# Kernel optimization log

Measured on AMD Instinct MI355X. Metric: run time of the kernel, lower is better.

Reference implementation:

```python
import jax, jax.numpy as jnp
import numpy as np

T_SCHEDULE = 999.0
LOG_2PI = float(np.log(2.0 * np.pi))


def setup_inputs() -> dict:
    key = jax.random.key(0)
    k1, k2, k3 = jax.random.split(key, 3)
    xt = jax.random.normal(k1, (128, 3, 32, 32), dtype=jnp.float32)
    # integer-style diffusion timesteps in [0, 900); divided by t_schedule=999 inside
    t = jax.random.uniform(k2, (128,), dtype=jnp.float32) * 900.0
    gt_images = jax.random.normal(k3, (20000, 3, 32, 32), dtype=jnp.float32)
    return {"xt": xt, "t": t, "gt_images": gt_images}


def reference(xt, t, gt_images):
    # AnalyticFlow.forward_fast
    B = xt.shape[0]
    N = gt_images.shape[0]
    x = jax.lax.stop_gradient(xt.reshape(B, -1))  # original detaches x
    gt = gt_images.reshape(N, -1)                 # [N, D]
    D = x.shape[-1]
    tt = t / T_SCHEDULE                           # [B]
    sig = 1.0 - tt                                # [B]
    # log N(term_2; 0, I) summed over D, where term_2 = (x - t*gt)/(1-t).
    # ||x - t*gt||^2 = ||x||^2 - 2 t x.gt + t^2 ||gt||^2  (avoids B*N*D tensor)
    x2 = jnp.sum(x * x, axis=-1)                  # [B]
    g2 = jnp.sum(gt * gt, axis=-1)                # [N]
    xg = x @ gt.T                                 # [B, N] GEMM
    sq = x2[:, None] - 2.0 * tt[:, None] * xg + (tt * tt)[:, None] * g2[None, :]
    log_p = -0.5 * sq / (sig * sig)[:, None] - 0.5 * D * LOG_2PI  # [B, N]
    log_p = log_p - jnp.max(log_p)                # global-max shift as in original
    eta = jax.nn.softmax(log_p, axis=1)           # [B, N], rows sum to 1
    # drift = mean_n (N*eta_n) * (gt_n - x)/(1-t) = (eta @ gt - x)/(1-t)
    drift = (eta @ gt - x) / sig[:, None]         # [B, D]
    return drift.reshape(xt.shape)
```

## Files before the change

kernel.cpp:

```cpp
#include <hip/hip_runtime.h>
#include <hip/hip_bf16.h>
#include <stdint.h>

#define B_SZ   128
#define D_SZ   3072
#define N_SZ   20000
#define NPAD   20480
#define BN     (B_SZ * NPAD)
#define BD     (B_SZ * D_SZ)

typedef __attribute__((ext_vector_type(8))) short        short8;
typedef __attribute__((ext_vector_type(4))) float        f32x4;
typedef __attribute__((ext_vector_type(2))) unsigned int uint2v;

__device__ __forceinline__ unsigned short f2bf(float f) {
    unsigned u = __float_as_uint(f);
    u += 0x7FFFu + ((u >> 16) & 1u);
    return (unsigned short)(u >> 16);
}
__device__ __forceinline__ float bf2f(unsigned short h) {
    return __uint_as_float(((unsigned)h) << 16);
}
__device__ __forceinline__ unsigned pk2bf(float a, float b) {
    __hip_bfloat162 h = __float22bfloat162_rn(make_float2(a, b));
    unsigned r;
    __builtin_memcpy(&r, &h, 4);
    return r;
}
__device__ __forceinline__ unsigned fkey_enc(float f) {
    unsigned b = __float_as_uint(f);
    return (b & 0x80000000u) ? ~b : (b | 0x80000000u);
}
__device__ __forceinline__ float fkey_dec(unsigned u) {
    return __uint_as_float((u & 0x80000000u) ? (u ^ 0x80000000u) : ~u);
}

__device__ __forceinline__ void gl_lds16(const void* g, void* l) {
    __builtin_amdgcn_global_load_lds(
        (const __attribute__((address_space(1))) void*)g,
        (__attribute__((address_space(3))) void*)l, 16, 0, 0);
}

__device__ __forceinline__ int swz(int r, int q) { return q ^ ((r >> 1) & 3); }

__global__ __launch_bounds__(256) void zero_small(float* __restrict__ p)
{
    p[blockIdx.x * 256 + threadIdx.x] = 0.f;
}

__global__ __launch_bounds__(256) void prep_x(const float* __restrict__ x,
                                              unsigned short* __restrict__ xhi,
                                              unsigned short* __restrict__ xlo)
{
    int i = blockIdx.x * 256 + threadIdx.x;
    float v = x[i];
    unsigned short h = f2bf(v);
    xhi[i] = h;
    xlo[i] = f2bf(v - bf2f(h));
}

__global__ __launch_bounds__(256) void scores_kernel(
        const float* __restrict__ gt,
        const unsigned short* __restrict__ xhi,
        const unsigned short* __restrict__ xlo,
        float* __restrict__ XG_part,
        float* __restrict__ G2)
{
    __shared__ __align__(16) unsigned short Xhi_t[128 * 32];
    __shared__ __align__(16) unsigned short Xlo_t[128 * 32];
    __shared__ __align__(16) unsigned short Ghi_t[64 * 32];
    __shared__ __align__(16) unsigned short Glo_t[64 * 32];

    const int tid   = threadIdx.x;
    const int kc    = blockIdx.x & 7;
    const int nt    = blockIdx.x >> 3;
    const int nbase = nt * 64;
    const int kcb   = kc * 384;

    const int lane = tid & 63;
    const int wave = tid >> 6;
    const int mh = wave & 1;
    const int nh = wave >> 1;
    const int lm = lane & 15;
    const int qd = lane >> 4;

    const int gn = tid >> 2;
    const int gq = tid & 3;
    const int ng0 = nbase + gn;
    int grow = ng0 > N_SZ - 1 ? N_SZ - 1 : ng0;
    const float* gp0 = gt + (size_t)grow * D_SZ + kcb + gq * 8;
    const int gwr = gn * 32 + swz(gn, gq) * 8;

    int xsrc[2], xdst[2];
    #pragma unroll
    for (int i = 0; i < 2; i++) {
        int o = (i * 256 + tid) * 16;
        int r = o >> 6;
        int j = (o >> 4) & 3;
        xdst[i] = o;
        xsrc[i] = r * D_SZ + kcb + swz(r, j) * 8;
    }

    float g2acc = 0.0f;

    f32x4 acc[4][2];
    #pragma unroll
    for (int i = 0; i < 4; i++)
        #pragma unroll
        for (int j = 0; j < 2; j++)
            acc[i][j] = (f32x4){0.f, 0.f, 0.f, 0.f};

    for (int k0 = 0; k0 < 384; k0 += 32) {
        #pragma unroll
        for (int i = 0; i < 2; i++) {
            gl_lds16(xhi + xsrc[i] + k0, (char*)Xhi_t + xdst[i]);
            gl_lds16(xlo + xsrc[i] + k0, (char*)Xlo_t + xdst[i]);
        }
        f32x4 v0 = *(const f32x4*)(gp0 + k0);
        f32x4 v1 = *(const f32x4*)(gp0 + k0 + 4);
        short8 h8, l8;
        #pragma unroll
        for (int j = 0; j < 4; j++) {
            float a = v0[j], b = v1[j];
            unsigned short ha = f2bf(a), hb = f2bf(b);
            h8[j]     = (short)ha;  h8[j + 4] = (short)hb;
            l8[j]     = (short)f2bf(a - bf2f(ha));
            l8[j + 4] = (short)f2bf(b - bf2f(hb));
            g2acc += a * a + b * b;
        }
        *(short8*)&Ghi_t[gwr] = h8;
        *(short8*)&Glo_t[gwr] = l8;

        __syncthreads();

        short8 bhi[2], blo[2];
        #pragma unroll
        for (int ni = 0; ni < 2; ni++) {
            int r = nh * 32 + ni * 16 + lm;
            int sl = r * 32 + swz(r, qd) * 8;
            bhi[ni] = *(short8*)&Ghi_t[sl];
            blo[ni] = *(short8*)&Glo_t[sl];
        }
        #pragma unroll
        for (int mi = 0; mi < 4; mi++) {
            int r = mh * 64 + mi * 16 + lm;
            int sl = r * 32 + swz(r, qd) * 8;
            short8 ahi = *(short8*)&Xhi_t[sl];
            short8 alo = *(short8*)&Xlo_t[sl];
            #pragma unroll
            for (int ni = 0; ni < 2; ni++) {
                acc[mi][ni] = __builtin_amdgcn_mfma_f32_16x16x32_bf16(ahi, bhi[ni], acc[mi][ni], 0, 0, 0);
                acc[mi][ni] = __builtin_amdgcn_mfma_f32_16x16x32_bf16(ahi, blo[ni], acc[mi][ni], 0, 0, 0);
                acc[mi][ni] = __builtin_amdgcn_mfma_f32_16x16x32_bf16(alo, bhi[ni], acc[mi][ni], 0, 0, 0);
            }
        }
        __syncthreads();
    }

    g2acc += __shfl_xor(g2acc, 1);
    g2acc += __shfl_xor(g2acc, 2);
    if (gq == 0 && ng0 < N_SZ) atomicAdd(&G2[ng0], g2acc);

    float* XGp = XG_part + (size_t)kc * BN;
    #pragma unroll
    for (int mi = 0; mi < 4; mi++) {
        #pragma unroll
        for (int ni = 0; ni < 2; ni++) {
            int ncol = nh * 32 + ni * 16 + lm;
            int ng = nbase + ncol;
            if (ng < N_SZ) {
                #pragma unroll
                for (int i = 0; i < 4; i++) {
                    int m = mh * 64 + mi * 16 + qd * 4 + i;
                    XGp[(size_t)m * NPAD + ng] = acc[mi][ni][i];
                }
            }
        }
    }
}

__global__ __launch_bounds__(256) void sum8(
        const float* __restrict__ XG_part, float* __restrict__ XG)
{
    int i = (blockIdx.x * 256 + threadIdx.x) * 4;
    f32x4 s = (f32x4){0.f, 0.f, 0.f, 0.f};
    #pragma unroll
    for (int kc = 0; kc < 8; kc++)
        s += *(const f32x4*)(XG_part + (size_t)kc * BN + i);
    *(f32x4*)(XG + i) = s;
}

__global__ __launch_bounds__(256) void maxk(
        const float* __restrict__ XG, const float* __restrict__ G2,
        const float* __restrict__ tarr, unsigned* __restrict__ Mkey)
{
    const int b  = blockIdx.x >> 3;
    const int ch = blockIdx.x & 7;
    const int tid = threadIdx.x;
    float tt  = tarr[b] / 999.0f;
    float sig = 1.0f - tt;
    float inv = 1.0f / (sig * sig);
    float c1 = tt * inv, c2 = 0.5f * tt * tt * inv;
    const float* xg = XG + (size_t)b * NPAD;
    __shared__ float wred[4];

    float mx = -3.402823466e+38f;
    int n0 = ch * 2560;
    for (int n = n0 + tid; n < n0 + 2560; n += 256)
        if (n < N_SZ) mx = fmaxf(mx, c1 * xg[n] - c2 * G2[n]);
    #pragma unroll
    for (int o = 32; o > 0; o >>= 1) mx = fmaxf(mx, __shfl_xor(mx, o));
    if ((tid & 63) == 0) wred[tid >> 6] = mx;
    __syncthreads();
    if (tid == 0) {
        mx = fmaxf(fmaxf(wred[0], wred[1]), fmaxf(wred[2], wred[3]));
        atomicMax(&Mkey[b], fkey_enc(mx));
    }
}

__global__ __launch_bounds__(256) void expk(
        const float* __restrict__ XG, const float* __restrict__ G2,
        const float* __restrict__ tarr, const unsigned* __restrict__ Mkey,
        unsigned short* __restrict__ P, float* __restrict__ L)
{
    const int b  = blockIdx.x >> 3;
    const int ch = blockIdx.x & 7;
    const int tid = threadIdx.x;
    float tt  = tarr[b] / 999.0f;
    float sig = 1.0f - tt;
    float inv = 1.0f / (sig * sig);
    float c1 = tt * inv, c2 = 0.5f * tt * tt * inv;
    float m = fkey_dec(Mkey[b]);
    const float* xg = XG + (size_t)b * NPAD;
    unsigned short* prow = P + (size_t)b * NPAD;
    __shared__ float wred[4];

    float sum = 0.f;
    int n0 = ch * 2560;
    for (int n = n0 + tid; n < n0 + 2560; n += 256) {
        float p = 0.f;
        if (n < N_SZ) { p = expf(c1 * xg[n] - c2 * G2[n] - m); sum += p; }
        prow[n] = f2bf(p);
    }
    #pragma unroll
    for (int o = 32; o > 0; o >>= 1) sum += __shfl_xor(sum, o);
    if ((tid & 63) == 0) wred[tid >> 6] = sum;
    __syncthreads();
    if (tid == 0) atomicAdd(&L[b], wred[0] + wred[1] + wred[2] + wred[3]);
}

__global__ __launch_bounds__(256) void drift_kernel(
        const float* __restrict__ gt,
        const unsigned short* __restrict__ P,
        float* __restrict__ Dacc_part)
{
    __shared__ __align__(16) unsigned short Pt[128 * 32];
    __shared__ __align__(16) unsigned short Gt[128 * 40];

    const int tid = threadIdx.x;
    const int nt = blockIdx.x % 24;
    const int kc = blockIdx.x / 24;
    const int dbase = nt * 128;

    const int lane = tid & 63;
    const int wave = tid >> 6;
    const int mh = wave & 1;
    const int dh = wave >> 1;
    const int lm = lane & 15;
    const int qd = lane >> 4;

    const int dg = tid & 31;
    const int kq = tid >> 5;

    int psrc[2], pdst[2];
    #pragma unroll
    for (int i = 0; i < 2; i++) {
        int o = (i * 256 + tid) * 16;
        int r = o >> 6;
        int j = (o >> 4) & 3;
        pdst[i] = o;
        psrc[i] = r * NPAD + kc * 512 + swz(r, j) * 8;
    }

    f32x4 acc[4][4];
    #pragma unroll
    for (int i = 0; i < 4; i++)
        #pragma unroll
        for (int j = 0; j < 4; j++)
            acc[i][j] = (f32x4){0.f, 0.f, 0.f, 0.f};

    for (int s = 0; s < 16; s++) {
        int kb = kc * 512 + s * 32;
        #pragma unroll
        for (int i = 0; i < 2; i++)
            gl_lds16(P + psrc[i] + s * 32, (char*)Pt + pdst[i]);
        f32x4 row[4];
        #pragma unroll
        for (int i = 0; i < 4; i++) {
            int kg = kb + kq * 4 + i;
            if (kg > N_SZ - 1) kg = N_SZ - 1;
            row[i] = *(const f32x4*)(gt + (size_t)kg * D_SZ + dbase + dg * 4);
        }
        #pragma unroll
        for (int j = 0; j < 4; j++) {
            unsigned u01 = pk2bf(row[0][j], row[1][j]);
            unsigned u23 = pk2bf(row[2][j], row[3][j]);
            uint2v pk = (uint2v){u01, u23};
            __builtin_memcpy((char*)Gt + (size_t)(dg * 4 + j) * 80 + kq * 8, &pk, 8);
        }
        __syncthreads();

        short8 af[4], bf8[4];
        #pragma unroll
        for (int mi = 0; mi < 4; mi++) {
            int r = mh * 64 + mi * 16 + lm;
            af[mi] = *(short8*)&Pt[r * 32 + swz(r, qd) * 8];
        }
        #pragma unroll
        for (int ni = 0; ni < 4; ni++)
            bf8[ni] = *(short8*)((char*)Gt + (size_t)(dh * 64 + ni * 16 + lm) * 80 + qd * 16);
        #pragma unroll
        for (int mi = 0; mi < 4; mi++)
            #pragma unroll
            for (int ni = 0; ni < 4; ni++)
                acc[mi][ni] = __builtin_amdgcn_mfma_f32_16x16x32_bf16(af[mi], bf8[ni], acc[mi][ni], 0, 0, 0);
        __syncthreads();
    }

    float* Dp = Dacc_part + (size_t)kc * BD;
    #pragma unroll
    for (int mi = 0; mi < 4; mi++)
        #pragma unroll
        for (int ni = 0; ni < 4; ni++) {
            int d = dbase + dh * 64 + ni * 16 + lm;
            #pragma unroll
            for (int i = 0; i < 4; i++) {
                int m = mh * 64 + mi * 16 + qd * 4 + i;
                Dp[(size_t)m * D_SZ + d] = acc[mi][ni][i];
            }
        }
}

__global__ __launch_bounds__(256) void epilogue_kernel(
        const float* __restrict__ Dacc_part, const float* __restrict__ L,
        const float* __restrict__ x, const float* __restrict__ tarr,
        float* __restrict__ out)
{
    int i = (blockIdx.x * 256 + threadIdx.x) * 4;
    int b = i / D_SZ;
    f32x4 s = (f32x4){0.f, 0.f, 0.f, 0.f};
    #pragma unroll
    for (int kc = 0; kc < 40; kc++)
        s += *(const f32x4*)(Dacc_part + (size_t)kc * BD + i);
    float tt = tarr[b] / 999.0f;
    float sig = 1.0f - tt;
    float invL = 1.0f / L[b];
    f32x4 xv = *(const f32x4*)(x + i);
    f32x4 o;
    #pragma unroll
    for (int j = 0; j < 4; j++) o[j] = (s[j] * invL - xv[j]) / sig;
    *(f32x4*)(out + i) = o;
}

extern "C" void kernel_launch(void* const* d_in, const int* in_sizes, int n_in,
                              void* d_out, int out_size, void* d_ws, size_t ws_size,
                              hipStream_t stream)
{
    const float* xt = (const float*)d_in[0];
    const float* t  = (const float*)d_in[1];
    const float* gt = (const float*)d_in[2];
    float* out = (float*)d_out;

    char* ws = (char*)d_ws;
    float*          XG_part  = (float*)(ws + 0);
    float*          XG       = (float*)(ws + 83886080);
    float*          Dacc_part= (float*)(ws + 94371840);
    float*          G2       = (float*)(ws + 157286400);
    unsigned*       Mkey     = (unsigned*)(ws + 157368320);
    float*          L        = (float*)(ws + 157368832);
    unsigned short* Xhi      = (unsigned short*)(ws + 157369344);
    unsigned short* Xlo      = (unsigned short*)(ws + 158155776);
    unsigned short* P        = (unsigned short*)(ws + 158942208);

    zero_small    <<<   81, 256, 0, stream>>>(G2);
    prep_x        <<< 1536, 256, 0, stream>>>(xt, Xhi, Xlo);
    scores_kernel <<< 2504, 256, 0, stream>>>(gt, Xhi, Xlo, XG_part, G2);
    sum8          <<< 2560, 256, 0, stream>>>(XG_part, XG);
    maxk          <<< 1024, 256, 0, stream>>>(XG, G2, t, Mkey);
    expk          <<< 1024, 256, 0, stream>>>(XG, G2, t, Mkey, P, L);
    drift_kernel  <<<  960, 256, 0, stream>>>(gt, P, Dacc_part);
    epilogue_kernel<<< 384, 256, 0, stream>>>(Dacc_part, L, xt, t, out);
}
```

Before: 486.4 us.

## Double-buffer LDS in scores and drift GEMMs and fuse split-K sum into max kernel

Both GEMM kernels now use ping-pong LDS buffers. The next K-slice's global loads are issued before the MFMA work on the current slice, and the converted data is written to the other buffer afterwards, so each step needs one barrier instead of two and memory latency is hidden behind compute. The separate sum8 kernel is removed. The split-K reduction of XG_part moves into maxk, which writes XG and computes the row max in the same pass, saving a launch and a full read/write of XG. Doubling LDS may lower occupancy, and the drift kernel's bf16 packing now uses a manual rounding helper in place of the intrinsic.

```diff
diff --git a/kernel.cpp b/kernel.cpp
--- a/kernel.cpp
+++ b/kernel.cpp
@@ -21,12 +21,6 @@
 __device__ __forceinline__ float bf2f(unsigned short h) {
     return __uint_as_float(((unsigned)h) << 16);
 }
-__device__ __forceinline__ unsigned pk2bf(float a, float b) {
-    __hip_bfloat162 h = __float22bfloat162_rn(make_float2(a, b));
-    unsigned r;
-    __builtin_memcpy(&r, &h, 4);
-    return r;
-}
 __device__ __forceinline__ unsigned fkey_enc(float f) {
     unsigned b = __float_as_uint(f);
     return (b & 0x80000000u) ? ~b : (b | 0x80000000u);
@@ -66,10 +60,10 @@
         float* __restrict__ XG_part,
         float* __restrict__ G2)
 {
-    __shared__ __align__(16) unsigned short Xhi_t[128 * 32];
-    __shared__ __align__(16) unsigned short Xlo_t[128 * 32];
-    __shared__ __align__(16) unsigned short Ghi_t[64 * 32];
-    __shared__ __align__(16) unsigned short Glo_t[64 * 32];
+    __shared__ __align__(16) unsigned short Xhi_t[2 * 128 * 32];
+    __shared__ __align__(16) unsigned short Xlo_t[2 * 128 * 32];
+    __shared__ __align__(16) unsigned short Ghi_t[2 * 64 * 32];
+    __shared__ __align__(16) unsigned short Glo_t[2 * 64 * 32];
 
     const int tid   = threadIdx.x;
     const int kc    = blockIdx.x & 7;
@@ -110,14 +104,14 @@
         for (int j = 0; j < 2; j++)
             acc[i][j] = (f32x4){0.f, 0.f, 0.f, 0.f};
 
-    for (int k0 = 0; k0 < 384; k0 += 32) {
+    {
         #pragma unroll
         for (int i = 0; i < 2; i++) {
-            gl_lds16(xhi + xsrc[i] + k0, (char*)Xhi_t + xdst[i]);
-            gl_lds16(xlo + xsrc[i] + k0, (char*)Xlo_t + xdst[i]);
-        }
-        f32x4 v0 = *(const f32x4*)(gp0 + k0);
-        f32x4 v1 = *(const f32x4*)(gp0 + k0 + 4);
+            gl_lds16(xhi + xsrc[i], (char*)Xhi_t + xdst[i]);
+            gl_lds16(xlo + xsrc[i], (char*)Xlo_t + xdst[i]);
+        }
+        f32x4 v0 = *(const f32x4*)(gp0);
+        f32x4 v1 = *(const f32x4*)(gp0 + 4);
         short8 h8, l8;
         #pragma unroll
         for (int j = 0; j < 4; j++) {
@@ -130,29 +124,64 @@
         }
         *(short8*)&Ghi_t[gwr] = h8;
         *(short8*)&Glo_t[gwr] = l8;
-
         __syncthreads();
-
-        short8 bhi[2], blo[2];
-        #pragma unroll
-        for (int ni = 0; ni < 2; ni++) {
-            int r = nh * 32 + ni * 16 + lm;
-            int sl = r * 32 + swz(r, qd) * 8;
-            bhi[ni] = *(short8*)&Ghi_t[sl];
-            blo[ni] = *(short8*)&Glo_t[sl];
-        }
-        #pragma unroll
-        for (int mi = 0; mi < 4; mi++) {
-            int r = mh * 64 + mi * 16 + lm;
-            int sl = r * 32 + swz(r, qd) * 8;
-            short8 ahi = *(short8*)&Xhi_t[sl];
-            short8 alo = *(short8*)&Xlo_t[sl];
+    }
+
+    for (int s = 0; s < 12; s++) {
+        const int cur = s & 1;
+        const int nxt = cur ^ 1;
+
+        f32x4 v0, v1;
+        if (s < 11) {
+            const int kn = (s + 1) * 32;
+            #pragma unroll
+            for (int i = 0; i < 2; i++) {
+                gl_lds16(xhi + xsrc[i] + kn, (char*)Xhi_t + nxt * 8192 + xdst[i]);
+                gl_lds16(xlo + xsrc[i] + kn, (char*)Xlo_t + nxt * 8192 + xdst[i]);
+            }
+            v0 = *(const f32x4*)(gp0 + kn);
+            v1 = *(const f32x4*)(gp0 + kn + 4);
+        }
+
+        {
+            const int xb = cur * 4096;
+            const int gb = cur * 2048;
+            short8 bhi[2], blo[2];
             #pragma unroll
             for (int ni = 0; ni < 2; ni++) {
-                acc[mi][ni] = __builtin_amdgcn_mfma_f32_16x16x32_bf16(ahi, bhi[ni], acc[mi][ni], 0, 0, 0);
-                acc[mi][ni] = __builtin_amdgcn_mfma_f32_16x16x32_bf16(ahi, blo[ni], acc[mi][ni], 0, 0, 0);
-                acc[mi][ni] = __builtin_amdgcn_mfma_f32_16x16x32_bf16(alo, bhi[ni], acc[mi][ni], 0, 0, 0);
-            }
+                int r = nh * 32 + ni * 16 + lm;
+                int sl = gb + r * 32 + swz(r, qd) * 8;
+                bhi[ni] = *(short8*)&Ghi_t[sl];
+                blo[ni] = *(short8*)&Glo_t[sl];
+            }
+            #pragma unroll
+            for (int mi = 0; mi < 4; mi++) {
+                int r = mh * 64 + mi * 16 + lm;
+                int sl = xb + r * 32 + swz(r, qd) * 8;
+                short8 ahi = *(short8*)&Xhi_t[sl];
+                short8 alo = *(short8*)&Xlo_t[sl];
+                #pragma unroll
+                for (int ni = 0; ni < 2; ni++) {
+                    acc[mi][ni] = __builtin_amdgcn_mfma_f32_16x16x32_bf16(ahi, bhi[ni], acc[mi][ni], 0, 0, 0);
+                    acc[mi][ni] = __builtin_amdgcn_mfma_f32_16x16x32_bf16(ahi, blo[ni], acc[mi][ni], 0, 0, 0);
+                    acc[mi][ni] = __builtin_amdgcn_mfma_f32_16x16x32_bf16(alo, bhi[ni], acc[mi][ni], 0, 0, 0);
+                }
+            }
+        }
+
+        if (s < 11) {
+            short8 h8, l8;
+            #pragma unroll
+            for (int j = 0; j < 4; j++) {
+                float a = v0[j], b = v1[j];
+                unsigned short ha = f2bf(a), hb = f2bf(b);
+                h8[j]     = (short)ha;  h8[j + 4] = (short)hb;
+                l8[j]     = (short)f2bf(a - bf2f(ha));
+                l8[j + 4] = (short)f2bf(b - bf2f(hb));
+                g2acc += a * a + b * b;
+            }
+            *(short8*)&Ghi_t[nxt * 2048 + gwr] = h8;
+            *(short8*)&Glo_t[nxt * 2048 + gwr] = l8;
         }
         __syncthreads();
     }
@@ -179,20 +208,10 @@
     }
 }
 
-__global__ __launch_bounds__(256) void sum8(
-        const float* __restrict__ XG_part, float* __restrict__ XG)
-{
-    int i = (blockIdx.x * 256 + threadIdx.x) * 4;
-    f32x4 s = (f32x4){0.f, 0.f, 0.f, 0.f};
-    #pragma unroll
-    for (int kc = 0; kc < 8; kc++)
-        s += *(const f32x4*)(XG_part + (size_t)kc * BN + i);
-    *(f32x4*)(XG + i) = s;
-}
-
 __global__ __launch_bounds__(256) void maxk(
-        const float* __restrict__ XG, const float* __restrict__ G2,
-        const float* __restrict__ tarr, unsigned* __restrict__ Mkey)
+        const float* __restrict__ XG_part, const float* __restrict__ G2,
+        const float* __restrict__ tarr, unsigned* __restrict__ Mkey,
+        float* __restrict__ XG)
 {
     const int b  = blockIdx.x >> 3;
     const int ch = blockIdx.x & 7;
@@ -201,13 +220,22 @@
     float sig = 1.0f - tt;
     float inv = 1.0f / (sig * sig);
     float c1 = tt * inv, c2 = 0.5f * tt * tt * inv;
-    const float* xg = XG + (size_t)b * NPAD;
     __shared__ float wred[4];
 
     float mx = -3.402823466e+38f;
     int n0 = ch * 2560;
-    for (int n = n0 + tid; n < n0 + 2560; n += 256)
-        if (n < N_SZ) mx = fmaxf(mx, c1 * xg[n] - c2 * G2[n]);
+    for (int n = n0 + tid * 4; n < n0 + 2560; n += 1024) {
+        f32x4 s = (f32x4){0.f, 0.f, 0.f, 0.f};
+        #pragma unroll
+        for (int kc = 0; kc < 8; kc++)
+            s += *(const f32x4*)(XG_part + (size_t)kc * BN + (size_t)b * NPAD + n);
+        *(f32x4*)(XG + (size_t)b * NPAD + n) = s;
+        #pragma unroll
+        for (int j = 0; j < 4; j++) {
+            int nn = n + j;
+            if (nn < N_SZ) mx = fmaxf(mx, c1 * s[j] - c2 * G2[nn]);
+        }
+    }
     #pragma unroll
     for (int o = 32; o > 0; o >>= 1) mx = fmaxf(mx, __shfl_xor(mx, o));
     if ((tid & 63) == 0) wred[tid >> 6] = mx;
@@ -254,8 +282,8 @@
         const unsigned short* __restrict__ P,
         float* __restrict__ Dacc_part)
 {
-    __shared__ __align__(16) unsigned short Pt[128 * 32];
-    __shared__ __align__(16) unsigned short Gt[128 * 40];
+    __shared__ __align__(16) unsigned short Pt[2 * 128 * 32];
+    __shared__ __align__(16) unsigned short Gt[2 * 128 * 40];
 
     const int tid = threadIdx.x;
     const int nt = blockIdx.x % 24;
@@ -289,41 +317,73 @@
         for (int j = 0; j < 4; j++)
             acc[i][j] = (f32x4){0.f, 0.f, 0.f, 0.f};
 
-    for (int s = 0; s < 16; s++) {
-        int kb = kc * 512 + s * 32;
+    {
         #pragma unroll
         for (int i = 0; i < 2; i++)
-            gl_lds16(P + psrc[i] + s * 32, (char*)Pt + pdst[i]);
+            gl_lds16(P + psrc[i], (char*)Pt + pdst[i]);
         f32x4 row[4];
         #pragma unroll
         for (int i = 0; i < 4; i++) {
-            int kg = kb + kq * 4 + i;
+            int kg = kc * 512 + kq * 4 + i;
             if (kg > N_SZ - 1) kg = N_SZ - 1;
             row[i] = *(const f32x4*)(gt + (size_t)kg * D_SZ + dbase + dg * 4);
         }
         #pragma unroll
         for (int j = 0; j < 4; j++) {
-            unsigned u01 = pk2bf(row[0][j], row[1][j]);
-            unsigned u23 = pk2bf(row[2][j], row[3][j]);
+            unsigned u01 = (unsigned)f2bf(row[0][j]) | ((unsigned)f2bf(row[1][j]) << 16);
+            unsigned u23 = (unsigned)f2bf(row[2][j]) | ((unsigned)f2bf(row[3][j]) << 16);
             uint2v pk = (uint2v){u01, u23};
             __builtin_memcpy((char*)Gt + (size_t)(dg * 4 + j) * 80 + kq * 8, &pk, 8);
         }
         __syncthreads();
-
-        short8 af[4], bf8[4];
-        #pragma unroll
-        for (int mi = 0; mi < 4; mi++) {
-            int r = mh * 64 + mi * 16 + lm;
-            af[mi] = *(short8*)&Pt[r * 32 + swz(r, qd) * 8];
-        }
-        #pragma unroll
-        for (int ni = 0; ni < 4; ni++)
-            bf8[ni] = *(short8*)((char*)Gt + (size_t)(dh * 64 + ni * 16 + lm) * 80 + qd * 16);
-        #pragma unroll
-        for (int mi = 0; mi < 4; mi++)
+    }
+
+    for (int s = 0; s < 16; s++) {
+        const int cur = s & 1;
+        const int nxt = cur ^ 1;
+
+        f32x4 row[4];
+        if (s < 15) {
+            #pragma unroll
+            for (int i = 0; i < 2; i++)
+                gl_lds16(P + psrc[i] + (s + 1) * 32, (char*)Pt + nxt * 8192 + pdst[i]);
+            int kb = kc * 512 + (s + 1) * 32;
+            #pragma unroll
+            for (int i = 0; i < 4; i++) {
+                int kg = kb + kq * 4 + i;
+                if (kg > N_SZ - 1) kg = N_SZ - 1;
+                row[i] = *(const f32x4*)(gt + (size_t)kg * D_SZ + dbase + dg * 4);
+            }
+        }
+
+        {
+            const int pb = cur * 4096;
+            const int gbB = cur * 10240;
+            short8 af[4], bf8[4];
+            #pragma unroll
+            for (int mi = 0; mi < 4; mi++) {
+                int r = mh * 64 + mi * 16 + lm;
+                af[mi] = *(short8*)&Pt[pb + r * 32 + swz(r, qd) * 8];
+            }
             #pragma unroll
             for (int ni = 0; ni < 4; ni++)
-                acc[mi][ni] = __builtin_amdgcn_mfma_f32_16x16x32_bf16(af[mi], bf8[ni], acc[mi][ni], 0, 0, 0);
+                bf8[ni] = *(short8*)((char*)Gt + gbB + (size_t)(dh * 64 + ni * 16 + lm) * 80 + qd * 16);
+            #pragma unroll
+            for (int mi = 0; mi < 4; mi++)
+                #pragma unroll
+                for (int ni = 0; ni < 4; ni++)
+                    acc[mi][ni] = __builtin_amdgcn_mfma_f32_16x16x32_bf16(af[mi], bf8[ni], acc[mi][ni], 0, 0, 0);
+        }
+
+        if (s < 15) {
+            #pragma unroll
+            for (int j = 0; j < 4; j++) {
+                unsigned u01 = (unsigned)f2bf(row[0][j]) | ((unsigned)f2bf(row[1][j]) << 16);
+                unsigned u23 = (unsigned)f2bf(row[2][j]) | ((unsigned)f2bf(row[3][j]) << 16);
+                uint2v pk = (uint2v){u01, u23};
+                __builtin_memcpy((char*)Gt + nxt * 10240 + (size_t)(dg * 4 + j) * 80 + kq * 8, &pk, 8);
+            }
+        }
         __syncthreads();
     }
 
@@ -385,8 +445,7 @@
     zero_small    <<<   81, 256, 0, stream>>>(G2);
     prep_x        <<< 1536, 256, 0, stream>>>(xt, Xhi, Xlo);
     scores_kernel <<< 2504, 256, 0, stream>>>(gt, Xhi, Xlo, XG_part, G2);
-    sum8          <<< 2560, 256, 0, stream>>>(XG_part, XG);
-    maxk          <<< 1024, 256, 0, stream>>>(XG, G2, t, Mkey);
+    maxk          <<< 1024, 256, 0, stream>>>(XG_part, G2, t, Mkey, XG);
     expk          <<< 1024, 256, 0, stream>>>(XG, G2, t, Mkey, P, L);
     drift_kernel  <<<  960, 256, 0, stream>>>(gt, P, Dacc_part);
     epilogue_kernel<<< 384, 256, 0, stream>>>(Dacc_part, L, xt, t, out);
```

After: 508.1 us. 4.5% more time.
